# Kernel optimization log

Hardware: AMD Instinct MI355X
Metric: run time of the kernel (lower is better)

## Reference

```python
import jax, jax.numpy as jnp
import numpy as np

N_USERS = 100000
EMBED = 128
N_EDGES = 1_600_000  # avg degree 16


def setup_inputs() -> dict:
    key = jax.random.key(0)
    k1, k2, k3, k4, k5 = jax.random.split(key, 5)
    s_rows = jnp.sort(jax.random.randint(k1, (N_EDGES,), 0, N_USERS))
    s_cols = jax.random.randint(k2, (N_EDGES,), 0, N_USERS)
    # row-normalization D^-1 A, matching the scipy preprocessing in __init__
    deg = jax.ops.segment_sum(jnp.ones((N_EDGES,), jnp.float32), s_rows, num_segments=N_USERS)
    deg = jnp.where(deg == 0, 1.0, deg)
    s_values = 1.0 / deg[s_rows]
    user_embeds = jax.random.normal(k3, (N_USERS, EMBED), jnp.float32) * 0.1
    bound = float(np.sqrt(6.0 / (EMBED + EMBED)))  # xavier_uniform
    W0 = jax.random.uniform(k4, (EMBED, EMBED), jnp.float32, -bound, bound)
    W1 = jax.random.uniform(k5, (EMBED, EMBED), jnp.float32, -bound, bound)
    return {"user_embeds": user_embeds, "s_rows": s_rows, "s_cols": s_cols,
            "s_values": s_values, "W0": W0, "W1": W1}


def reference(user_embeds, s_rows, s_cols, s_values, W0, W1):
    # SocialGCN.forward: per layer x_new = x + dropout(S @ (x @ W_l));
    # dropout is identity in eval mode. Returns all layer outputs (stacked).
    n_users = user_embeds.shape[0]
    outs = [user_embeds]
    x = user_embeds
    for W in (W0, W1):
        xt = x @ W  # [n_users, d] dense GEMM
        # SpMM: out[r] = sum_{e: rows[e]==r} vals[e] * xt[cols[e]]
        msg = s_values[:, None] * xt[s_cols]  # [n_edges, d] irregular gather
        agg = jax.ops.segment_sum(msg, s_rows, num_segments=n_users)
        x = x + agg  # residual add
        outs.append(x)
    return jnp.stack(outs)  # [n_layers+1, n_users, d]
```

## Files before the change

kernel.cpp:

```cpp
#include <hip/hip_runtime.h>

#define N_USERS 100000
#define EMBED   128

typedef __attribute__((ext_vector_type(8))) short bf16x8;
typedef __attribute__((ext_vector_type(4))) float f32x4;
typedef __attribute__((ext_vector_type(4))) uint  u32x4;

__global__ __launch_bounds__(256) void rowptr_kernel(const int* __restrict__ rows,
                                                     int* __restrict__ row_ptr,
                                                     int n_rows, int n_edges) {
  int r = blockIdx.x * blockDim.x + threadIdx.x;
  if (r > n_rows) return;
  int lo = 0, hi = n_edges;
  while (lo < hi) {
    int mid = (lo + hi) >> 1;
    if (rows[mid] < r) lo = mid + 1; else hi = mid;
  }
  row_ptr[r] = lo;
}

__global__ __launch_bounds__(256) void wconv_kernel(const float* __restrict__ W0,
                                                    const float* __restrict__ W1,
                                                    uint* __restrict__ Wt0,
                                                    uint* __restrict__ Wt1) {
  const float* W  = blockIdx.x ? W1 : W0;
  uint*        Wt = blockIdx.x ? Wt1 : Wt0;
  for (int idx = threadIdx.x; idx < 128 * 64; idx += 256) {
    int n = idx >> 6;
    int kp = idx & 63;
    float a = W[(2 * kp) * 128 + n];
    float b = W[(2 * kp + 1) * 128 + n];
    uint o;
    asm("v_cvt_pk_bf16_f32 %0, %1, %2" : "=v"(o) : "v"(a), "v"(b));
    Wt[n * 64 + kp] = o;
  }
}

#define XS_STRIDE 136

__global__ __launch_bounds__(256) void gemm_kernel(const float* __restrict__ X,
                                                   const ushort* __restrict__ Wt,
                                                   ushort* __restrict__ Y,
                                                   float* __restrict__ Xcopy) {
  __shared__ ushort Xs[64 * XS_STRIDE];
  const int tid  = threadIdx.x;
  const int wave = tid >> 6;
  const int lane = tid & 63;
  const int l15  = lane & 15;
  const int lg   = lane >> 4;
  const int row0 = blockIdx.x * 64;

  #pragma unroll
  for (int i = 0; i < 8; ++i) {
    int idx4 = i * 256 + tid;
    int r    = idx4 >> 5;
    int kc   = idx4 & 31;
    int gr   = row0 + r;
    int grc  = gr < N_USERS ? gr : N_USERS - 1;
    float4 v = *(const float4*)(X + (size_t)grc * EMBED + kc * 4);
    if (Xcopy && gr < N_USERS)
      *(float4*)(Xcopy + (size_t)gr * EMBED + kc * 4) = v;
    uint2 p;
    asm("v_cvt_pk_bf16_f32 %0, %1, %2" : "=v"(p.x) : "v"(v.x), "v"(v.y));
    asm("v_cvt_pk_bf16_f32 %0, %1, %2" : "=v"(p.y) : "v"(v.z), "v"(v.w));
    *(uint2*)(Xs + r * XS_STRIDE + kc * 4) = p;
  }
  __syncthreads();

  const int tr = wave * 16 + l15;
  const int m  = row0 + tr;

  f32x4 acc[8];
  #pragma unroll
  for (int t = 0; t < 8; ++t) acc[t] = (f32x4){0.f, 0.f, 0.f, 0.f};

  #pragma unroll
  for (int s = 0; s < 4; ++s) {
    const int k0 = s * 32 + lg * 8;
    union { bf16x8 v; uint4 u; } bfr;
    bfr.u = *(const uint4*)(Xs + tr * XS_STRIDE + k0);
    #pragma unroll
    for (int nt = 0; nt < 8; ++nt) {
      union { bf16x8 v; uint4 u; } afr;
      afr.u = *(const uint4*)(Wt + (size_t)(nt * 16 + l15) * 128 + k0);
      acc[nt] = __builtin_amdgcn_mfma_f32_16x16x32_bf16(afr.v, bfr.v, acc[nt], 0, 0, 0);
    }
  }

  if (m < N_USERS) {
    ushort* yrow = Y + (size_t)m * EMBED;
    #pragma unroll
    for (int nt = 0; nt < 8; ++nt) {
      uint2 o;
      asm("v_cvt_pk_bf16_f32 %0, %1, %2" : "=v"(o.x) : "v"(acc[nt][0]), "v"(acc[nt][1]));
      asm("v_cvt_pk_bf16_f32 %0, %1, %2" : "=v"(o.y) : "v"(acc[nt][2]), "v"(acc[nt][3]));
      *(uint2*)(yrow + nt * 16 + lg * 4) = o;
    }
  }
}

__device__ __forceinline__ void fma8(float* acc, u32x4 g, float v) {
  acc[0] = fmaf(v, __uint_as_float(g[0] << 16),         acc[0]);
  acc[1] = fmaf(v, __uint_as_float(g[0] & 0xffff0000u), acc[1]);
  acc[2] = fmaf(v, __uint_as_float(g[1] << 16),         acc[2]);
  acc[3] = fmaf(v, __uint_as_float(g[1] & 0xffff0000u), acc[3]);
  acc[4] = fmaf(v, __uint_as_float(g[2] << 16),         acc[4]);
  acc[5] = fmaf(v, __uint_as_float(g[2] & 0xffff0000u), acc[5]);
  acc[6] = fmaf(v, __uint_as_float(g[3] << 16),         acc[6]);
  acc[7] = fmaf(v, __uint_as_float(g[3] & 0xffff0000u), acc[7]);
}

__global__ __launch_bounds__(256) void spmm_kernel(const ushort* __restrict__ XT,
                                                   const float* __restrict__ X,
                                                   const int* __restrict__ row_ptr,
                                                   const int* __restrict__ cols,
                                                   const float* __restrict__ vals,
                                                   float* __restrict__ OUT) {
  const int tid = threadIdx.x;
  const int l   = tid & 15;
  const int rg  = tid >> 4;
  const int row = blockIdx.x * 16 + rg;
  if (row >= N_USERS) return;
  const int start = row_ptr[row];
  const int end   = row_ptr[row + 1];
  const u32x4* XT4 = (const u32x4*)XT;

  float acc[8];
  {
    float4 r0 = *(const float4*)(X + (size_t)row * EMBED + l * 8);
    float4 r1 = *(const float4*)(X + (size_t)row * EMBED + l * 8 + 4);
    acc[0] = r0.x; acc[1] = r0.y; acc[2] = r0.z; acc[3] = r0.w;
    acc[4] = r1.x; acc[5] = r1.y; acc[6] = r1.z; acc[7] = r1.w;
  }

  int e = start;
  int e_pre = (start + 3) & ~3;
  if (e_pre > end) e_pre = end;
  for (; e < e_pre; ++e) {
    u32x4 g = XT4[(size_t)cols[e] * 16 + l];
    fma8(acc, g, vals[e]);
  }
  for (; e + 8 <= end; e += 8) {
    int4   ca = *(const int4*)(cols + e);
    int4   cb = *(const int4*)(cols + e + 4);
    float4 va = *(const float4*)(vals + e);
    float4 vb = *(const float4*)(vals + e + 4);
    u32x4 g0 = XT4[(size_t)ca.x * 16 + l];
    u32x4 g1 = XT4[(size_t)ca.y * 16 + l];
    u32x4 g2 = XT4[(size_t)ca.z * 16 + l];
    u32x4 g3 = XT4[(size_t)ca.w * 16 + l];
    u32x4 g4 = XT4[(size_t)cb.x * 16 + l];
    u32x4 g5 = XT4[(size_t)cb.y * 16 + l];
    u32x4 g6 = XT4[(size_t)cb.z * 16 + l];
    u32x4 g7 = XT4[(size_t)cb.w * 16 + l];
    fma8(acc, g0, va.x); fma8(acc, g1, va.y);
    fma8(acc, g2, va.z); fma8(acc, g3, va.w);
    fma8(acc, g4, vb.x); fma8(acc, g5, vb.y);
    fma8(acc, g6, vb.z); fma8(acc, g7, vb.w);
  }
  for (; e + 4 <= end; e += 4) {
    int4   ca = *(const int4*)(cols + e);
    float4 va = *(const float4*)(vals + e);
    u32x4 g0 = XT4[(size_t)ca.x * 16 + l];
    u32x4 g1 = XT4[(size_t)ca.y * 16 + l];
    u32x4 g2 = XT4[(size_t)ca.z * 16 + l];
    u32x4 g3 = XT4[(size_t)ca.w * 16 + l];
    fma8(acc, g0, va.x); fma8(acc, g1, va.y);
    fma8(acc, g2, va.z); fma8(acc, g3, va.w);
  }
  for (; e < end; ++e) {
    u32x4 g = XT4[(size_t)cols[e] * 16 + l];
    fma8(acc, g, vals[e]);
  }

  float4 o0 = {acc[0], acc[1], acc[2], acc[3]};
  float4 o1 = {acc[4], acc[5], acc[6], acc[7]};
  *(float4*)(OUT + (size_t)row * EMBED + l * 8)     = o0;
  *(float4*)(OUT + (size_t)row * EMBED + l * 8 + 4) = o1;
}

extern "C" void kernel_launch(void* const* d_in, const int* in_sizes, int n_in,
                              void* d_out, int out_size, void* d_ws, size_t ws_size,
                              hipStream_t stream) {
  const float* user_embeds = (const float*)d_in[0];
  const int*   s_rows      = (const int*)d_in[1];
  const int*   s_cols      = (const int*)d_in[2];
  const float* s_values    = (const float*)d_in[3];
  const float* W0          = (const float*)d_in[4];
  const float* W1          = (const float*)d_in[5];
  float* out = (float*)d_out;

  const int n_edges = in_sizes[1];
  const size_t layer = (size_t)N_USERS * EMBED;

  char* ws = (char*)d_ws;
  ushort* xt      = (ushort*)ws;   ws += layer * sizeof(ushort);
  ushort* Wt0     = (ushort*)ws;   ws += 128 * 128 * sizeof(ushort);
  ushort* Wt1     = (ushort*)ws;   ws += 128 * 128 * sizeof(ushort);
  int*    row_ptr = (int*)ws;

  rowptr_kernel<<<(N_USERS + 1 + 255) / 256, 256, 0, stream>>>(
      s_rows, row_ptr, N_USERS, n_edges);
  wconv_kernel<<<2, 256, 0, stream>>>(W0, W1, (uint*)Wt0, (uint*)Wt1);

  const ushort* Wtl[2] = {Wt0, Wt1};
  for (int l = 0; l < 2; ++l) {
    const float* Xl = (l == 0) ? user_embeds : (out + l * layer);
    gemm_kernel<<<(N_USERS + 63) / 64, 256, 0, stream>>>(
        Xl, Wtl[l], xt, l == 0 ? out : nullptr);
    spmm_kernel<<<(N_USERS + 15) / 16, 256, 0, stream>>>(
        xt, Xl, row_ptr, s_cols, s_values, out + (l + 1) * layer);
  }
}
```

Measured before the change: 245.8 us.

## Bucket each row's edges by column range and load GEMM inputs directly

Adds a preprocessing kernel that reorders each row's edges into 8 column-range buckets, so SpMM gathers at any moment tend to hit a narrower region of the XT table and get more cache reuse. The GEMM drops its shared-memory staging and has each lane read its own X row straight from global memory, converting to bf16 in registers. The 8-edge unrolled SpMM loop is also removed. The bucket kernel is a serial, divergent per-thread pass over each row's edges, 8 times over, and it costs extra workspace.

New measurement: 317.5 us. 29.1% more time.

```diff
diff --git a/kernel.cpp b/kernel.cpp
--- a/kernel.cpp
+++ b/kernel.cpp
@@ -1,7 +1,9 @@
 #include <hip/hip_runtime.h>
 
-#define N_USERS 100000
-#define EMBED   128
+#define N_USERS  100000
+#define EMBED    128
+#define NPHASE   8
+#define BUCKETW  12500
 
 typedef __attribute__((ext_vector_type(8))) short bf16x8;
 typedef __attribute__((ext_vector_type(4))) float f32x4;
@@ -18,6 +20,24 @@
     if (rows[mid] < r) lo = mid + 1; else hi = mid;
   }
   row_ptr[r] = lo;
+}
+
+__global__ __launch_bounds__(256) void bucket_kernel(const int* __restrict__ row_ptr,
+                                                     const int* __restrict__ cols,
+                                                     const float* __restrict__ vals,
+                                                     int* __restrict__ cols2,
+                                                     float* __restrict__ vals2) {
+  int r = blockIdx.x * blockDim.x + threadIdx.x;
+  if (r >= N_USERS) return;
+  const int s = row_ptr[r], e = row_ptr[r + 1];
+  int w = s;
+  #pragma unroll
+  for (int p = 0; p < NPHASE; ++p) {
+    for (int i = s; i < e; ++i) {
+      int c = cols[i];
+      if (c / BUCKETW == p) { cols2[w] = c; vals2[w] = vals[i]; ++w; }
+    }
+  }
 }
 
 __global__ __launch_bounds__(256) void wconv_kernel(const float* __restrict__ W0,
@@ -37,39 +57,19 @@
   }
 }
 
-#define XS_STRIDE 136
-
 __global__ __launch_bounds__(256) void gemm_kernel(const float* __restrict__ X,
                                                    const ushort* __restrict__ Wt,
                                                    ushort* __restrict__ Y,
                                                    float* __restrict__ Xcopy) {
-  __shared__ ushort Xs[64 * XS_STRIDE];
   const int tid  = threadIdx.x;
   const int wave = tid >> 6;
   const int lane = tid & 63;
   const int l15  = lane & 15;
   const int lg   = lane >> 4;
-  const int row0 = blockIdx.x * 64;
-
-  #pragma unroll
-  for (int i = 0; i < 8; ++i) {
-    int idx4 = i * 256 + tid;
-    int r    = idx4 >> 5;
-    int kc   = idx4 & 31;
-    int gr   = row0 + r;
-    int grc  = gr < N_USERS ? gr : N_USERS - 1;
-    float4 v = *(const float4*)(X + (size_t)grc * EMBED + kc * 4);
-    if (Xcopy && gr < N_USERS)
-      *(float4*)(Xcopy + (size_t)gr * EMBED + kc * 4) = v;
-    uint2 p;
-    asm("v_cvt_pk_bf16_f32 %0, %1, %2" : "=v"(p.x) : "v"(v.x), "v"(v.y));
-    asm("v_cvt_pk_bf16_f32 %0, %1, %2" : "=v"(p.y) : "v"(v.z), "v"(v.w));
-    *(uint2*)(Xs + r * XS_STRIDE + kc * 4) = p;
-  }
-  __syncthreads();
-
-  const int tr = wave * 16 + l15;
-  const int m  = row0 + tr;
+  const int m    = blockIdx.x * 64 + wave * 16 + l15;
+  const int mc   = m < N_USERS ? m : N_USERS - 1;
+  const bool act = m < N_USERS;
+  const float* xrow = X + (size_t)mc * EMBED;
 
   f32x4 acc[8];
   #pragma unroll
@@ -78,8 +78,17 @@
   #pragma unroll
   for (int s = 0; s < 4; ++s) {
     const int k0 = s * 32 + lg * 8;
-    union { bf16x8 v; uint4 u; } bfr;
-    bfr.u = *(const uint4*)(Xs + tr * XS_STRIDE + k0);
+    float4 xa = *(const float4*)(xrow + k0);
+    float4 xb = *(const float4*)(xrow + k0 + 4);
+    if (Xcopy && act) {
+      *(float4*)(Xcopy + (size_t)m * EMBED + k0)     = xa;
+      *(float4*)(Xcopy + (size_t)m * EMBED + k0 + 4) = xb;
+    }
+    union { bf16x8 v; uint u[4]; } bfr;
+    asm("v_cvt_pk_bf16_f32 %0, %1, %2" : "=v"(bfr.u[0]) : "v"(xa.x), "v"(xa.y));
+    asm("v_cvt_pk_bf16_f32 %0, %1, %2" : "=v"(bfr.u[1]) : "v"(xa.z), "v"(xa.w));
+    asm("v_cvt_pk_bf16_f32 %0, %1, %2" : "=v"(bfr.u[2]) : "v"(xb.x), "v"(xb.y));
+    asm("v_cvt_pk_bf16_f32 %0, %1, %2" : "=v"(bfr.u[3]) : "v"(xb.z), "v"(xb.w));
     #pragma unroll
     for (int nt = 0; nt < 8; ++nt) {
       union { bf16x8 v; uint4 u; } afr;
@@ -88,7 +97,7 @@
     }
   }
 
-  if (m < N_USERS) {
+  if (act) {
     ushort* yrow = Y + (size_t)m * EMBED;
     #pragma unroll
     for (int nt = 0; nt < 8; ++nt) {
@@ -141,24 +150,6 @@
     u32x4 g = XT4[(size_t)cols[e] * 16 + l];
     fma8(acc, g, vals[e]);
   }
-  for (; e + 8 <= end; e += 8) {
-    int4   ca = *(const int4*)(cols + e);
-    int4   cb = *(const int4*)(cols + e + 4);
-    float4 va = *(const float4*)(vals + e);
-    float4 vb = *(const float4*)(vals + e + 4);
-    u32x4 g0 = XT4[(size_t)ca.x * 16 + l];
-    u32x4 g1 = XT4[(size_t)ca.y * 16 + l];
-    u32x4 g2 = XT4[(size_t)ca.z * 16 + l];
-    u32x4 g3 = XT4[(size_t)ca.w * 16 + l];
-    u32x4 g4 = XT4[(size_t)cb.x * 16 + l];
-    u32x4 g5 = XT4[(size_t)cb.y * 16 + l];
-    u32x4 g6 = XT4[(size_t)cb.z * 16 + l];
-    u32x4 g7 = XT4[(size_t)cb.w * 16 + l];
-    fma8(acc, g0, va.x); fma8(acc, g1, va.y);
-    fma8(acc, g2, va.z); fma8(acc, g3, va.w);
-    fma8(acc, g4, vb.x); fma8(acc, g5, vb.y);
-    fma8(acc, g6, vb.z); fma8(acc, g7, vb.w);
-  }
   for (; e + 4 <= end; e += 4) {
     int4   ca = *(const int4*)(cols + e);
     float4 va = *(const float4*)(vals + e);
@@ -195,14 +186,18 @@
   const size_t layer = (size_t)N_USERS * EMBED;
 
   char* ws = (char*)d_ws;
-  ushort* xt      = (ushort*)ws;   ws += layer * sizeof(ushort);
-  ushort* Wt0     = (ushort*)ws;   ws += 128 * 128 * sizeof(ushort);
-  ushort* Wt1     = (ushort*)ws;   ws += 128 * 128 * sizeof(ushort);
-  int*    row_ptr = (int*)ws;
+  ushort* xt      = (ushort*)ws;  ws += layer * sizeof(ushort);
+  ushort* Wt0     = (ushort*)ws;  ws += 128 * 128 * sizeof(ushort);
+  ushort* Wt1     = (ushort*)ws;  ws += 128 * 128 * sizeof(ushort);
+  int*    row_ptr = (int*)ws;     ws += (N_USERS + 1) * sizeof(int) + 12;
+  int*    cols2   = (int*)ws;     ws += (size_t)n_edges * sizeof(int);
+  float*  vals2   = (float*)ws;
 
   rowptr_kernel<<<(N_USERS + 1 + 255) / 256, 256, 0, stream>>>(
       s_rows, row_ptr, N_USERS, n_edges);
   wconv_kernel<<<2, 256, 0, stream>>>(W0, W1, (uint*)Wt0, (uint*)Wt1);
+  bucket_kernel<<<(N_USERS + 255) / 256, 256, 0, stream>>>(
+      row_ptr, s_cols, s_values, cols2, vals2);
 
   const ushort* Wtl[2] = {Wt0, Wt1};
   for (int l = 0; l < 2; ++l) {
@@ -210,6 +205,6 @@
     gemm_kernel<<<(N_USERS + 63) / 64, 256, 0, stream>>>(
         Xl, Wtl[l], xt, l == 0 ? out : nullptr);
     spmm_kernel<<<(N_USERS + 15) / 16, 256, 0, stream>>>(
-        xt, Xl, row_ptr, s_cols, s_values, out + (l + 1) * layer);
-  }
-}
+        xt, Xl, row_ptr, cols2, vals2, out + (l + 1) * layer);
+  }
+}
```
